# Performance work log

Hardware: AMD Instinct MI355X
Metric: run time of the kernel (lower is better)

## Reference

```python
import jax, jax.numpy as jnp
import numpy as np

NU, NI = 4000, 4000
R, M, OUT = 5, 256, 75
SIDE, FDIM = 64, 128


def setup_inputs() -> dict:
    key = jax.random.key(0)
    ks = jax.random.split(key, 12)
    return {
        "adj_matrix": jax.random.randint(ks[0], (NU, NI), 0, 6, dtype=jnp.int32),
        "u_sideFeat": jax.random.normal(ks[1], (NU, FDIM), dtype=jnp.float32),
        "v_sideFeat": jax.random.normal(ks[2], (NI, FDIM), dtype=jnp.float32),
        "msg_W": jax.random.normal(ks[3], (R, M, NU + NI), dtype=jnp.float32) * 0.05,
        "dense_W": jax.random.normal(ks[4], (OUT, M), dtype=jnp.float32) * 0.05,
        "u_W1": jax.random.normal(ks[5], (SIDE, FDIM), dtype=jnp.float32) * 0.05,
        "u_b1": jax.random.normal(ks[6], (SIDE,), dtype=jnp.float32) * 0.05,
        "u_W2": jax.random.normal(ks[7], (OUT, SIDE), dtype=jnp.float32) * 0.05,
        "v_W1": jax.random.normal(ks[8], (SIDE, FDIM), dtype=jnp.float32) * 0.05,
        "v_b1": jax.random.normal(ks[9], (SIDE,), dtype=jnp.float32) * 0.05,
        "v_W2": jax.random.normal(ks[10], (OUT, SIDE), dtype=jnp.float32) * 0.05,
        "isNegative": 0,
    }


def reference(adj_matrix, u_sideFeat, v_sideFeat, msg_W, dense_W,
              u_W1, u_b1, u_W2, v_W1, v_b1, v_W2, isNegative):
    # isNegative=0, dropout=0 -> one-hot matrices are exact identity slices,
    # so msgLayer(sum_j adj_r[i,j]/C * onehot_j) == (adj_r/C) @ W_r[:, cols].T
    nu, ni = adj_matrix.shape
    r_vals = jnp.arange(1, msg_W.shape[0] + 1, dtype=adj_matrix.dtype)
    # rating-split binary adjacencies [R, NU, NI]
    A = (adj_matrix[None, :, :] == r_vals[:, None, None]).astype(jnp.float32)
    Nu = A.sum(axis=(0, 2))            # user degree over all ratings [NU]
    Nv = A.sum(axis=(0, 1))            # item degree [NI]
    C = jnp.sqrt(Nu[:, None] * Nv[None, :])  # symmetric normalization [NU, NI]
    Csafe = jnp.where(C > 0, C, 1.0)
    An = A / Csafe[None, :, :]
    W_users = msg_W[:, :, :nu]         # [R, M, NU]
    W_items = msg_W[:, :, nu:]         # [R, M, NI]
    # accum='sum' over ratings, then relu
    Hu = jax.nn.relu(jnp.einsum('rui,rmi->um', An, W_items))  # [NU, M]
    Hv = jax.nn.relu(jnp.einsum('rui,rmu->im', An, W_users))  # [NI, M]
    Fu = jax.nn.relu(u_sideFeat @ u_W1.T + u_b1)
    Fv = jax.nn.relu(v_sideFeat @ v_W1.T + v_b1)
    U = jax.nn.relu(Hu @ dense_W.T + Fu @ u_W2.T)
    V = jax.nn.relu(Hv @ dense_W.T + Fv @ v_W2.T)
    return (U, V)
```

## Files before the change

### kernel.cpp

```cpp
#include <hip/hip_runtime.h>
#include <hip/hip_bf16.h>
#include <stdint.h>

#define NU 4000
#define NI 4000
#define RR 5
#define MM 256
#define OUTD 75
#define FDIM 128
#define KP 4096
#define KPH 2048
#define HP_STRIDE 1024000

typedef float f32x4 __attribute__((ext_vector_type(4)));
typedef int   i32x4 __attribute__((ext_vector_type(4)));
typedef short bf16x8 __attribute__((ext_vector_type(8)));

static __device__ __forceinline__ short f2b(float x) {
  __hip_bfloat16 h = __float2bfloat16(x);
  return (short)__builtin_bit_cast(unsigned short, h);
}
static __device__ __forceinline__ float b2f(short x) {
  unsigned int u = ((unsigned int)(unsigned short)x) << 16;
  return __builtin_bit_cast(float, u);
}
static __device__ __forceinline__ bf16x8 cvt8(f32x4 a, f32x4 b) {
  bf16x8 r;
  r[0] = f2b(a[0]); r[1] = f2b(a[1]); r[2] = f2b(a[2]); r[3] = f2b(a[3]);
  r[4] = f2b(b[0]); r[5] = f2b(b[1]); r[6] = f2b(b[2]); r[7] = f2b(b[3]);
  return r;
}

__global__ __launch_bounds__(256) void k_trans(const int* __restrict__ adj,
                                               uint8_t* __restrict__ a8p,
                                               uint8_t* __restrict__ a8tp,
                                               int* __restrict__ Nu,
                                               int* __restrict__ Nv) {
  __shared__ int8_t lt[64][65];
  __shared__ int rowc[64];
  __shared__ int colp[4][64];
  const int i0 = blockIdx.x * 64;
  const int u0 = blockIdx.y * 64;
  const int t = threadIdx.x;
  const int w = t >> 6, lane = t & 63;
  int mycol = 0;
  for (int rep = 0; rep < 16; rep++) {
    const int r = rep * 4 + w;
    const int u = u0 + r, i = i0 + lane;
    int a = (u < NU && i < NI) ? adj[(size_t)u * NI + i] : 0;
    const int nz = (a > 0) ? 1 : 0;
    unsigned long long bal = __ballot(nz);
    if (lane == 0) rowc[r] = (int)__popcll(bal);
    mycol += nz;
    lt[lane][r] = (int8_t)a;
    const int nb = __shfl_down(a, 1);
    if (!(lane & 1))
      a8p[(size_t)u * KPH + (i0 >> 1) + (lane >> 1)] = (uint8_t)(a | (nb << 4));
  }
  colp[w][lane] = mycol;
  __syncthreads();
  for (int rep = 0; rep < 16; rep++) {
    const int r = rep * 4 + w;
    const int it = i0 + r;
    const int v = lt[r][lane];
    const int nb = __shfl_down(v, 1);
    if (!(lane & 1))
      a8tp[(size_t)it * KPH + (u0 >> 1) + (lane >> 1)] = (uint8_t)(v | (nb << 4));
  }
  if (t < 64) {
    const int cc = colp[0][t] + colp[1][t] + colp[2][t] + colp[3][t];
    if (i0 + t < NI && cc) atomicAdd(&Nv[i0 + t], cc);
    if (u0 + t < NU && rowc[t]) atomicAdd(&Nu[u0 + t], rowc[t]);
  }
}

__global__ __launch_bounds__(256) void k_pbuild(const float* __restrict__ msgW,
                                                const int* __restrict__ Nu,
                                                const int* __restrict__ Nv,
                                                int8_t* __restrict__ Pu,
                                                int8_t* __restrict__ Pv) {
  const int b = blockIdx.x;
  const float* src = msgW + (size_t)b * (NU + NI);
#pragma unroll
  for (int it = 0; it < 2; ++it) {
    const int base = (threadIdx.x + it * 256) * 8;
    uint32_t lou = 0, hiu = 0, lov = 0, hiv = 0;
    if (base < NU) {
      const f32x4 v0 = *(const f32x4*)(src + base);
      const f32x4 v1 = *(const f32x4*)(src + base + 4);
      const f32x4 u0 = *(const f32x4*)(src + NU + base);
      const f32x4 u1 = *(const f32x4*)(src + NU + base + 4);
      const int4 cu0 = *(const int4*)(Nu + base);
      const int4 cu1 = *(const int4*)(Nu + base + 4);
      const int4 cv0 = *(const int4*)(Nv + base);
      const int4 cv1 = *(const int4*)(Nv + base + 4);
      float qv[8], qu[8];
      const int cus[8] = {cu0.x, cu0.y, cu0.z, cu0.w, cu1.x, cu1.y, cu1.z, cu1.w};
      const int cvs[8] = {cv0.x, cv0.y, cv0.z, cv0.w, cv1.x, cv1.y, cv1.z, cv1.w};
      const float vs[8] = {v0[0], v0[1], v0[2], v0[3], v1[0], v1[1], v1[2], v1[3]};
      const float us[8] = {u0[0], u0[1], u0[2], u0[3], u1[0], u1[1], u1[2], u1[3]};
#pragma unroll
      for (int j = 0; j < 8; ++j) {
        const float su = cus[j] > 0 ? rsqrtf((float)cus[j]) * 256.0f : 0.f;
        const float sv = cvs[j] > 0 ? rsqrtf((float)cvs[j]) * 256.0f : 0.f;
        qv[j] = fminf(fmaxf(vs[j] * su, -127.f), 127.f);
        qu[j] = fminf(fmaxf(us[j] * sv, -127.f), 127.f);
      }
      uint32_t bv[8], bu[8];
#pragma unroll
      for (int j = 0; j < 8; ++j) {
        bv[j] = (uint32_t)(uint8_t)(int8_t)__float2int_rn(qv[j]);
        bu[j] = (uint32_t)(uint8_t)(int8_t)__float2int_rn(qu[j]);
      }
      lov = bv[0] | (bv[2] << 8) | (bv[4] << 16) | (bv[6] << 24);
      hiv = bv[1] | (bv[3] << 8) | (bv[5] << 16) | (bv[7] << 24);
      lou = bu[0] | (bu[2] << 8) | (bu[4] << 16) | (bu[6] << 24);
      hiu = bu[1] | (bu[3] << 8) | (bu[5] << 16) | (bu[7] << 24);
    }
    *(uint2*)(Pv + (size_t)b * KP + base) = make_uint2(lov, hiv);
    *(uint2*)(Pu + (size_t)b * KP + base) = make_uint2(lou, hiu);
  }
}

#define GLOAD_LDS(g, s) __builtin_amdgcn_global_load_lds( \
    (const __attribute__((address_space(1))) uint32_t*)(g), \
    (__attribute__((address_space(3))) uint32_t*)(s), 16, 0, 0)

static __device__ __forceinline__ uint32_t ohp(uint32_t sel, int r) {
  const uint32_t TL[5] = {0x00000100u, 0x00010000u, 0x01000000u, 0u, 0u};
  const uint32_t TH[5] = {0u, 0u, 0u, 0x00000001u, 0x00000100u};
  return __builtin_amdgcn_perm(TH[r], TL[r], sel);
}

__global__ __launch_bounds__(256, 5) void k_gemm(const uint8_t* __restrict__ Au,
                                                 const uint8_t* __restrict__ Av,
                                                 const int8_t* __restrict__ Pu,
                                                 const int8_t* __restrict__ Pv,
                                                 const int* __restrict__ Nu,
                                                 const int* __restrict__ Nv,
                                                 __hip_bfloat16* __restrict__ Hp) {
  __shared__ __attribute__((aligned(16))) char Bls[2][10240];

  const int bid = blockIdx.x;
  const int side = bid & 1;
  const int bn = (bid >> 1) & 7;
  const int rest = bid >> 4;
  const int ks = rest % 5;
  const int bm = rest / 5;
  const uint8_t* __restrict__ A8 = side ? Av : Au;
  const int8_t* __restrict__ P  = side ? Pv : Pu;
  const int* __restrict__ cnt = side ? Nv : Nu;
  const int kbeg = ks * 832;
  const int nst = (ks == 4) ? 12 : 13;

  const int t = threadIdx.x;
  const int w = t >> 6, l = t & 63;
  const int l15 = l & 15, l4 = l >> 4;

  const int scnt = (w < 2) ? 3 : 2;
  const int nb = (w < 2) ? w * 3 : 6 + (w - 2) * 2;
  uint32_t soff[3], ldst[3];
  {
    const uint32_t jsrc = (uint32_t)((l & 3) ^ ((l >> 3) & 3));
#pragma unroll
    for (int i = 0; i < 3; ++i) {
      const int n = nb + ((i < scnt) ? i : 0);
      const int r = n >> 1, chunk = n & 1;
      const int colg = bn * 32 + chunk * 16 + (l >> 2);
      soff[i] = (uint32_t)(r * 256 + colg) * KP + jsrc * 16u;
      ldst[i] = (uint32_t)(n << 10);
    }
  }
#define STAGE(bi, kk) { \
  GLOAD_LDS(P + soff[0] + (uint32_t)(kk), &Bls[bi][0] + ldst[0]); \
  GLOAD_LDS(P + soff[1] + (uint32_t)(kk), &Bls[bi][0] + ldst[1]); \
  if (scnt == 3) GLOAD_LDS(P + soff[2] + (uint32_t)(kk), &Bls[bi][0] + ldst[2]); }

  const uint32_t rbase = (uint32_t)(l15 * 64) +
                         ((uint32_t)(l4 ^ ((l15 >> 1) & 3)) << 4);

  uint32_t paoff[4];
#pragma unroll
  for (int g = 0; g < 4; ++g)
    paoff[g] = (uint32_t)(bm * 256 + w * 64 + g * 16 + l15) * KPH + l4 * 8;

  i32x4 acc[4][2] = {};
  uint2 aC[4], aN[4];

  STAGE(0, kbeg);
#pragma unroll
  for (int g = 0; g < 4; ++g)
    aC[g] = *(const uint2*)(A8 + paoff[g] + (kbeg >> 1));
  __syncthreads();

  for (int st = 0; st < nst; ++st) {
    const int kk = kbeg + st * 64;
    if (st + 1 < nst) {
      STAGE((st & 1) ^ 1, kk + 64);
#pragma unroll
      for (int g = 0; g < 4; ++g)
        aN[g] = *(const uint2*)(A8 + paoff[g] + ((kk + 64) >> 1));
    }
    uint32_t ud[4][4];
#pragma unroll
    for (int g = 0; g < 4; ++g) {
      ud[g][0] = aC[g].x & 0x0F0F0F0Fu;
      ud[g][1] = (aC[g].x >> 4) & 0x0F0F0F0Fu;
      ud[g][2] = aC[g].y & 0x0F0F0F0Fu;
      ud[g][3] = (aC[g].y >> 4) & 0x0F0F0F0Fu;
    }
    const char* lb = &Bls[st & 1][0];
#pragma unroll
    for (int r = 0; r < 5; ++r) {
      const uint4 B0 = *(const uint4*)(lb + r * 2048 + rbase);
      const uint4 B1 = *(const uint4*)(lb + r * 2048 + rbase + 1024);
#pragma unroll
      for (int g = 0; g < 4; ++g) {
        uint4 af;
        af.x = ohp(ud[g][0], r); af.y = ohp(ud[g][1], r);
        af.z = ohp(ud[g][2], r); af.w = ohp(ud[g][3], r);
        const i32x4 a4 = __builtin_bit_cast(i32x4, af);
        acc[g][0] = __builtin_amdgcn_mfma_i32_16x16x64_i8(
            a4, __builtin_bit_cast(i32x4, B0), acc[g][0], 0, 0, 0);
        acc[g][1] = __builtin_amdgcn_mfma_i32_16x16x64_i8(
            a4, __builtin_bit_cast(i32x4, B1), acc[g][1], 0, 0, 0);
      }
    }
#pragma unroll
    for (int g = 0; g < 4; ++g) aC[g] = aN[g];
    __syncthreads();
  }

  __hip_bfloat16* hp = Hp + (size_t)(ks * 2 + side) * HP_STRIDE;
#pragma unroll
  for (int g = 0; g < 4; ++g) {
    const int rowb = bm * 256 + w * 64 + g * 16 + l4 * 4;
#pragma unroll
    for (int c = 0; c < 2; ++c) {
      const int ocol = bn * 32 + c * 16 + l15;
#pragma unroll
      for (int q = 0; q < 4; ++q) {
        const int orow = rowb + q;
        if (orow < 4000) {
          const int cv = cnt[orow];
          const float s = cv > 0 ? rsqrtf((float)cv) * (1.0f / 256.0f) : 0.f;
          hp[(size_t)orow * 256 + ocol] = __float2bfloat16((float)acc[g][c][q] * s);
        }
      }
    }
  }
#undef STAGE
}

__global__ __launch_bounds__(64) void k_out(const __hip_bfloat16* __restrict__ Hp,
                                            const float* __restrict__ usf,
                                            const float* __restrict__ vsf,
                                            const float* __restrict__ dW,
                                            const float* __restrict__ uW1,
                                            const float* __restrict__ ub1,
                                            const float* __restrict__ uW2,
                                            const float* __restrict__ vW1,
                                            const float* __restrict__ vb1,
                                            const float* __restrict__ vW2,
                                            float* __restrict__ out) {
  const int bid = blockIdx.x;
  const int side = bid / 250, rb = bid % 250;
  const int l = threadIdx.x & 63;
  const int l15 = l & 15, l4 = l >> 4;
  const int r0 = rb * 16;
  const float* __restrict__ sf = side ? vsf : usf;
  const float* __restrict__ W1 = side ? vW1 : uW1;
  const float* __restrict__ b1 = side ? vb1 : ub1;
  const float* __restrict__ W2 = side ? vW2 : uW2;
  const __hip_bfloat16* __restrict__ hp = Hp + (size_t)side * HP_STRIDE;

  const int myrow = r0 + l15;

  __shared__ __hip_bfloat16 lf[16][72];

  f32x4 fA[4] = {};
#pragma unroll
  for (int kk = 0; kk < 128; kk += 32) {
    const float* ps = sf + (size_t)myrow * 128 + kk + 8 * l4;
    const bf16x8 af = cvt8(*(const f32x4*)ps, *(const f32x4*)(ps + 4));
#pragma unroll
    for (int c = 0; c < 4; ++c) {
      const float* pw = W1 + (size_t)(c * 16 + l15) * 128 + kk + 8 * l4;
      const bf16x8 bf = cvt8(*(const f32x4*)pw, *(const f32x4*)(pw + 4));
      fA[c] = __builtin_amdgcn_mfma_f32_16x16x32_bf16(af, bf, fA[c], 0, 0, 0);
    }
  }
#pragma unroll
  for (int c = 0; c < 4; ++c) {
    const float bv = b1[c * 16 + l15];
#pragma unroll
    for (int reg = 0; reg < 4; ++reg) {
      float v = fA[c][reg] + bv;
      lf[l4 * 4 + reg][c * 16 + l15] = __float2bfloat16(v > 0.f ? v : 0.f);
    }
  }
  __syncthreads();

  f32x4 oA[5] = {};
  const __hip_bfloat16* hbase = hp + (size_t)myrow * 256 + 8 * l4;
#pragma unroll
  for (int kk = 0; kk < 256; kk += 32) {
    const bf16x8 q0 = *(const bf16x8*)(hbase + kk);
    const bf16x8 q1 = *(const bf16x8*)(hbase + 2 * HP_STRIDE + kk);
    const bf16x8 q2 = *(const bf16x8*)(hbase + 4 * HP_STRIDE + kk);
    const bf16x8 q3 = *(const bf16x8*)(hbase + 6 * HP_STRIDE + kk);
    const bf16x8 q4 = *(const bf16x8*)(hbase + 8 * HP_STRIDE + kk);
    bf16x8 af;
#pragma unroll
    for (int j = 0; j < 8; ++j) {
      float hv = b2f(q0[j]) + b2f(q1[j]) + b2f(q2[j]) + b2f(q3[j]) + b2f(q4[j]);
      af[j] = f2b(hv > 0.f ? hv : 0.f);
    }
#pragma unroll
    for (int c = 0; c < 5; ++c) {
      int oc = c * 16 + l15; if (oc > 74) oc = 74;
      const float* pd = dW + (size_t)oc * 256 + kk + 8 * l4;
      const bf16x8 bf = cvt8(*(const f32x4*)pd, *(const f32x4*)(pd + 4));
      oA[c] = __builtin_amdgcn_mfma_f32_16x16x32_bf16(af, bf, oA[c], 0, 0, 0);
    }
  }
#pragma unroll
  for (int kk = 0; kk < 64; kk += 32) {
    const bf16x8 af = *(const bf16x8*)(&lf[l15][kk + 8 * l4]);
#pragma unroll
    for (int c = 0; c < 5; ++c) {
      int oc = c * 16 + l15; if (oc > 74) oc = 74;
      const float* pw = W2 + (size_t)oc * 64 + kk + 8 * l4;
      const bf16x8 bf = cvt8(*(const f32x4*)pw, *(const f32x4*)(pw + 4));
      oA[c] = __builtin_amdgcn_mfma_f32_16x16x32_bf16(af, bf, oA[c], 0, 0, 0);
    }
  }
  float* po = out + (size_t)side * (4000 * 75);
#pragma unroll
  for (int c = 0; c < 5; ++c) {
    const int oc = c * 16 + l15;
    if (oc < 75) {
#pragma unroll
      for (int reg = 0; reg < 4; ++reg) {
        const int orow = r0 + l4 * 4 + reg;
        const float v = oA[c][reg];
        po[(size_t)orow * 75 + oc] = v > 0.f ? v : 0.f;
      }
    }
  }
}

extern "C" void kernel_launch(void* const* d_in, const int* in_sizes, int n_in,
                              void* d_out, int out_size, void* d_ws, size_t ws_size,
                              hipStream_t stream) {
  const int* adj = (const int*)d_in[0];
  const float* usf = (const float*)d_in[1];
  const float* vsf = (const float*)d_in[2];
  const float* msgW = (const float*)d_in[3];
  const float* dW = (const float*)d_in[4];
  const float* uW1 = (const float*)d_in[5];
  const float* ub1 = (const float*)d_in[6];
  const float* uW2 = (const float*)d_in[7];
  const float* vW1 = (const float*)d_in[8];
  const float* vb1 = (const float*)d_in[9];
  const float* vW2 = (const float*)d_in[10];
  float* out = (float*)d_out;

  char* w = (char*)d_ws;
  const size_t A_BYTES = (size_t)4096 * KPH;
  const size_t P_BYTES = (size_t)RR * MM * KP;
  const size_t HP_BYTES = (size_t)10 * HP_STRIDE * 2;
  int* Nu = (int*)w;
  int* Nv = (int*)(w + 16384);
  uint8_t* Au = (uint8_t*)(w + 32768);
  uint8_t* Av = Au + A_BYTES;
  int8_t* Pu = (int8_t*)(w + 32768 + 2 * A_BYTES);
  int8_t* Pv = Pu + P_BYTES;
  __hip_bfloat16* Hp = (__hip_bfloat16*)(w + 32768 + 2 * A_BYTES + 2 * P_BYTES);
  const size_t need = 32768 + 2 * A_BYTES + 2 * P_BYTES + HP_BYTES;
  if (ws_size < need) return;

  hipMemsetAsync(w, 0, 32768, stream);
  k_trans<<<dim3(64, 64), 256, 0, stream>>>(adj, Au, Av, Nu, Nv);
  k_pbuild<<<1280, 256, 0, stream>>>(msgW, Nu, Nv, Pu, Pv);
  k_gemm<<<1280, 256, 0, stream>>>(Au, Av, Pu, Pv, Nu, Nv, Hp);
  k_out<<<500, 64, 0, stream>>>(Hp, usf, vsf, dW, uW1, ub1, uW2, vW1, vb1, vW2,
                                out);
}
```

Baseline: 103.5 us.

## Switch int8 GEMM to 32x32x32 MFMA and split K six ways

The adjacency GEMM now uses 32x32x32 int8 MFMA tiles instead of 16x16x64, with a matching LDS staging layout and fragment mapping. The K dimension is split into six partitions instead of five, which raises the grid to 1536 blocks, and the output kernel sums six partial buffers. The larger MFMA shape is meant to cut instruction count and LDS reads per FLOP, and the extra split is meant to fill more CUs. In exchange it uses more workspace, writes and reads one more partial buffer, and unpacks the bf16 fragments differently.

```diff
diff --git a/kernel.cpp b/kernel.cpp
--- a/kernel.cpp
+++ b/kernel.cpp
@@ -14,6 +14,7 @@
 
 typedef float f32x4 __attribute__((ext_vector_type(4)));
 typedef int   i32x4 __attribute__((ext_vector_type(4)));
+typedef int   i32x16 __attribute__((ext_vector_type(16)));
 typedef short bf16x8 __attribute__((ext_vector_type(8)));
 
 static __device__ __forceinline__ short f2b(float x) {
@@ -132,7 +133,7 @@
   return __builtin_amdgcn_perm(TH[r], TL[r], sel);
 }
 
-__global__ __launch_bounds__(256, 5) void k_gemm(const uint8_t* __restrict__ Au,
+__global__ __launch_bounds__(256, 6) void k_gemm(const uint8_t* __restrict__ Au,
                                                  const uint8_t* __restrict__ Av,
                                                  const int8_t* __restrict__ Pu,
                                                  const int8_t* __restrict__ Pv,
@@ -145,52 +146,49 @@
   const int side = bid & 1;
   const int bn = (bid >> 1) & 7;
   const int rest = bid >> 4;
-  const int ks = rest % 5;
-  const int bm = rest / 5;
+  const int ks = rest % 6;
+  const int bm = rest / 6;
   const uint8_t* __restrict__ A8 = side ? Av : Au;
   const int8_t* __restrict__ P  = side ? Pv : Pu;
   const int* __restrict__ cnt = side ? Nv : Nu;
-  const int kbeg = ks * 832;
-  const int nst = (ks == 4) ? 12 : 13;
+  const int kbeg = (ks < 4) ? ks * 704 : 2816 + (ks - 4) * 640;
+  const int nst = (ks < 4) ? 11 : 10;
 
   const int t = threadIdx.x;
   const int w = t >> 6, l = t & 63;
-  const int l15 = l & 15, l4 = l >> 4;
+  const int l31 = l & 31, lh = l >> 5;
 
   const int scnt = (w < 2) ? 3 : 2;
   const int nb = (w < 2) ? w * 3 : 6 + (w - 2) * 2;
   uint32_t soff[3], ldst[3];
-  {
-    const uint32_t jsrc = (uint32_t)((l & 3) ^ ((l >> 3) & 3));
-#pragma unroll
-    for (int i = 0; i < 3; ++i) {
-      const int n = nb + ((i < scnt) ? i : 0);
-      const int r = n >> 1, chunk = n & 1;
-      const int colg = bn * 32 + chunk * 16 + (l >> 2);
-      soff[i] = (uint32_t)(r * 256 + colg) * KP + jsrc * 16u;
-      ldst[i] = (uint32_t)(n << 10);
-    }
+#pragma unroll
+  for (int i = 0; i < 3; ++i) {
+    const int n = nb + ((i < scnt) ? i : 0);
+    const int r = n >> 1, h = n & 1;
+    soff[i] = (uint32_t)((r * 256 + bn * 32 + l31) * KP) +
+              (uint32_t)(lh * 32 + h * 16);
+    ldst[i] = (uint32_t)(n << 10);
   }
 #define STAGE(bi, kk) { \
   GLOAD_LDS(P + soff[0] + (uint32_t)(kk), &Bls[bi][0] + ldst[0]); \
   GLOAD_LDS(P + soff[1] + (uint32_t)(kk), &Bls[bi][0] + ldst[1]); \
   if (scnt == 3) GLOAD_LDS(P + soff[2] + (uint32_t)(kk), &Bls[bi][0] + ldst[2]); }
 
-  const uint32_t rbase = (uint32_t)(l15 * 64) +
-                         ((uint32_t)(l4 ^ ((l15 >> 1) & 3)) << 4);
-
-  uint32_t paoff[4];
-#pragma unroll
-  for (int g = 0; g < 4; ++g)
-    paoff[g] = (uint32_t)(bm * 256 + w * 64 + g * 16 + l15) * KPH + l4 * 8;
-
-  i32x4 acc[4][2] = {};
-  uint2 aC[4], aN[4];
+  const uint32_t rb2 = (uint32_t)(lh * 512 + l31 * 16);
+
+  uint32_t paoff[2];
+#pragma unroll
+  for (int g = 0; g < 2; ++g)
+    paoff[g] = (uint32_t)(bm * 256 + w * 64 + g * 32 + l31) * KPH + lh * 16;
+
+  i32x16 acc[2] = {};
+  uint4 aC[2], aN[2];
 
   STAGE(0, kbeg);
 #pragma unroll
-  for (int g = 0; g < 4; ++g)
-    aC[g] = *(const uint2*)(A8 + paoff[g] + (kbeg >> 1));
+  for (int g = 0; g < 2; ++g)
+    aC[g] = *(const uint4*)(A8 + paoff[g] + (kbeg >> 1));
+  aN[0] = aC[0]; aN[1] = aC[1];
   __syncthreads();
 
   for (int st = 0; st < nst; ++st) {
@@ -198,54 +196,57 @@
     if (st + 1 < nst) {
       STAGE((st & 1) ^ 1, kk + 64);
 #pragma unroll
-      for (int g = 0; g < 4; ++g)
-        aN[g] = *(const uint2*)(A8 + paoff[g] + ((kk + 64) >> 1));
-    }
-    uint32_t ud[4][4];
-#pragma unroll
-    for (int g = 0; g < 4; ++g) {
+      for (int g = 0; g < 2; ++g)
+        aN[g] = *(const uint4*)(A8 + paoff[g] + ((kk + 64) >> 1));
+    }
+    uint32_t ud[2][8];
+#pragma unroll
+    for (int g = 0; g < 2; ++g) {
       ud[g][0] = aC[g].x & 0x0F0F0F0Fu;
       ud[g][1] = (aC[g].x >> 4) & 0x0F0F0F0Fu;
       ud[g][2] = aC[g].y & 0x0F0F0F0Fu;
       ud[g][3] = (aC[g].y >> 4) & 0x0F0F0F0Fu;
+      ud[g][4] = aC[g].z & 0x0F0F0F0Fu;
+      ud[g][5] = (aC[g].z >> 4) & 0x0F0F0F0Fu;
+      ud[g][6] = aC[g].w & 0x0F0F0F0Fu;
+      ud[g][7] = (aC[g].w >> 4) & 0x0F0F0F0Fu;
     }
     const char* lb = &Bls[st & 1][0];
 #pragma unroll
     for (int r = 0; r < 5; ++r) {
-      const uint4 B0 = *(const uint4*)(lb + r * 2048 + rbase);
-      const uint4 B1 = *(const uint4*)(lb + r * 2048 + rbase + 1024);
-#pragma unroll
-      for (int g = 0; g < 4; ++g) {
-        uint4 af;
-        af.x = ohp(ud[g][0], r); af.y = ohp(ud[g][1], r);
-        af.z = ohp(ud[g][2], r); af.w = ohp(ud[g][3], r);
-        const i32x4 a4 = __builtin_bit_cast(i32x4, af);
-        acc[g][0] = __builtin_amdgcn_mfma_i32_16x16x64_i8(
-            a4, __builtin_bit_cast(i32x4, B0), acc[g][0], 0, 0, 0);
-        acc[g][1] = __builtin_amdgcn_mfma_i32_16x16x64_i8(
-            a4, __builtin_bit_cast(i32x4, B1), acc[g][1], 0, 0, 0);
-      }
-    }
-#pragma unroll
-    for (int g = 0; g < 4; ++g) aC[g] = aN[g];
+      const uint4 B0 = *(const uint4*)(lb + r * 2048 + rb2);
+      const uint4 B1 = *(const uint4*)(lb + r * 2048 + 1024 + rb2);
+#pragma unroll
+      for (int g = 0; g < 2; ++g) {
+        uint4 a0, a1;
+        a0.x = ohp(ud[g][0], r); a0.y = ohp(ud[g][1], r);
+        a0.z = ohp(ud[g][2], r); a0.w = ohp(ud[g][3], r);
+        acc[g] = __builtin_amdgcn_mfma_i32_32x32x32_i8(
+            __builtin_bit_cast(i32x4, a0), __builtin_bit_cast(i32x4, B0),
+            acc[g], 0, 0, 0);
+        a1.x = ohp(ud[g][4], r); a1.y = ohp(ud[g][5], r);
+        a1.z = ohp(ud[g][6], r); a1.w = ohp(ud[g][7], r);
+        acc[g] = __builtin_amdgcn_mfma_i32_32x32x32_i8(
+            __builtin_bit_cast(i32x4, a1), __builtin_bit_cast(i32x4, B1),
+            acc[g], 0, 0, 0);
+      }
+    }
+    aC[0] = aN[0]; aC[1] = aN[1];
     __syncthreads();
   }
 
   __hip_bfloat16* hp = Hp + (size_t)(ks * 2 + side) * HP_STRIDE;
-#pragma unroll
-  for (int g = 0; g < 4; ++g) {
-    const int rowb = bm * 256 + w * 64 + g * 16 + l4 * 4;
-#pragma unroll
-    for (int c = 0; c < 2; ++c) {
-      const int ocol = bn * 32 + c * 16 + l15;
-#pragma unroll
-      for (int q = 0; q < 4; ++q) {
-        const int orow = rowb + q;
-        if (orow < 4000) {
-          const int cv = cnt[orow];
-          const float s = cv > 0 ? rsqrtf((float)cv) * (1.0f / 256.0f) : 0.f;
-          hp[(size_t)orow * 256 + ocol] = __float2bfloat16((float)acc[g][c][q] * s);
-        }
+  const int ocol = bn * 32 + l31;
+#pragma unroll
+  for (int g = 0; g < 2; ++g) {
+    const int rowb = bm * 256 + w * 64 + g * 32 + 4 * lh;
+#pragma unroll
+    for (int reg = 0; reg < 16; ++reg) {
+      const int orow = rowb + (reg & 3) + 8 * (reg >> 2);
+      if (orow < 4000) {
+        const int cv = cnt[orow];
+        const float s = cv > 0 ? rsqrtf((float)cv) * (1.0f / 256.0f) : 0.f;
+        hp[(size_t)orow * 256 + ocol] = __float2bfloat16((float)acc[g][reg] * s);
       }
     }
   }
@@ -310,10 +311,12 @@
     const bf16x8 q2 = *(const bf16x8*)(hbase + 4 * HP_STRIDE + kk);
     const bf16x8 q3 = *(const bf16x8*)(hbase + 6 * HP_STRIDE + kk);
     const bf16x8 q4 = *(const bf16x8*)(hbase + 8 * HP_STRIDE + kk);
+    const bf16x8 q5 = *(const bf16x8*)(hbase + 10 * HP_STRIDE + kk);
     bf16x8 af;
 #pragma unroll
     for (int j = 0; j < 8; ++j) {
-      float hv = b2f(q0[j]) + b2f(q1[j]) + b2f(q2[j]) + b2f(q3[j]) + b2f(q4[j]);
+      float hv = b2f(q0[j]) + b2f(q1[j]) + b2f(q2[j]) + b2f(q3[j]) +
+                 b2f(q4[j]) + b2f(q5[j]);
       af[j] = f2b(hv > 0.f ? hv : 0.f);
     }
 #pragma unroll
@@ -369,7 +372,7 @@
   char* w = (char*)d_ws;
   const size_t A_BYTES = (size_t)4096 * KPH;
   const size_t P_BYTES = (size_t)RR * MM * KP;
-  const size_t HP_BYTES = (size_t)10 * HP_STRIDE * 2;
+  const size_t HP_BYTES = (size_t)12 * HP_STRIDE * 2;
   int* Nu = (int*)w;
   int* Nv = (int*)(w + 16384);
   uint8_t* Au = (uint8_t*)(w + 32768);
@@ -383,7 +386,7 @@
   hipMemsetAsync(w, 0, 32768, stream);
   k_trans<<<dim3(64, 64), 256, 0, stream>>>(adj, Au, Av, Nu, Nv);
   k_pbuild<<<1280, 256, 0, stream>>>(msgW, Nu, Nv, Pu, Pv);
-  k_gemm<<<1280, 256, 0, stream>>>(Au, Av, Pu, Pv, Nu, Nv, Hp);
+  k_gemm<<<1536, 256, 0, stream>>>(Au, Av, Pu, Pv, Nu, Nv, Hp);
   k_out<<<500, 64, 0, stream>>>(Hp, usf, vsf, dW, uW1, ub1, uW2, vW1, vb1, vW2,
                                 out);
 }
```

Result: slower. 110.2 us (+6.5%).

## Vectorize nibble packing in transpose and split output kernel across four waves

Applied to the files above, without the earlier changes.

The transpose kernel now stages both the row and transposed tiles in shared memory and packs nibbles with wide 32-bit perm operations and 8-byte stores, replacing per-lane shuffles and byte stores. A new pre-kernel converts the dense and side-feature weights to bf16 once, with padded rows, so the output kernel no longer converts fp32 weights inside its loops. The output kernel moves from one wave per 16 rows to four waves per 32 rows. The side-feature MLP and half of the dense K-loop run concurrently in separate waves, and the partial sums are combined through shared memory. This adds a launch, two barriers and extra shared memory in exchange for better overlap and occupancy in the small tail stages.

```diff
diff --git a/kernel.cpp b/kernel.cpp
--- a/kernel.cpp
+++ b/kernel.cpp
@@ -36,7 +36,8 @@
                                                uint8_t* __restrict__ a8tp,
                                                int* __restrict__ Nu,
                                                int* __restrict__ Nv) {
-  __shared__ int8_t lt[64][65];
+  __shared__ int8_t lp[64][68];
+  __shared__ int8_t lt[64][68];
   __shared__ int rowc[64];
   __shared__ int colp[4][64];
   const int i0 = blockIdx.x * 64;
@@ -52,20 +53,26 @@
     unsigned long long bal = __ballot(nz);
     if (lane == 0) rowc[r] = (int)__popcll(bal);
     mycol += nz;
+    lp[r][lane] = (int8_t)a;
     lt[lane][r] = (int8_t)a;
-    const int nb = __shfl_down(a, 1);
-    if (!(lane & 1))
-      a8p[(size_t)u * KPH + (i0 >> 1) + (lane >> 1)] = (uint8_t)(a | (nb << 4));
   }
   colp[w][lane] = mycol;
   __syncthreads();
-  for (int rep = 0; rep < 16; rep++) {
-    const int r = rep * 4 + w;
-    const int it = i0 + r;
-    const int v = lt[r][lane];
-    const int nb = __shfl_down(v, 1);
-    if (!(lane & 1))
-      a8tp[(size_t)it * KPH + (u0 >> 1) + (lane >> 1)] = (uint8_t)(v | (nb << 4));
+  {
+    const int r = t >> 2, c = t & 3;
+    const uint32_t* xp = (const uint32_t*)(&lp[r][c * 16]);
+    const uint32_t* xt = (const uint32_t*)(&lt[r][c * 16]);
+    uint32_t t0, t1, t2, t3, w0, w1;
+    t0 = xp[0] | (xp[0] >> 4); t1 = xp[1] | (xp[1] >> 4);
+    t2 = xp[2] | (xp[2] >> 4); t3 = xp[3] | (xp[3] >> 4);
+    w0 = __builtin_amdgcn_perm(t1, t0, 0x06040200u);
+    w1 = __builtin_amdgcn_perm(t3, t2, 0x06040200u);
+    *(uint2*)(a8p + (size_t)(u0 + r) * KPH + (i0 >> 1) + c * 8) = make_uint2(w0, w1);
+    t0 = xt[0] | (xt[0] >> 4); t1 = xt[1] | (xt[1] >> 4);
+    t2 = xt[2] | (xt[2] >> 4); t3 = xt[3] | (xt[3] >> 4);
+    w0 = __builtin_amdgcn_perm(t1, t0, 0x06040200u);
+    w1 = __builtin_amdgcn_perm(t3, t2, 0x06040200u);
+    *(uint2*)(a8tp + (size_t)(i0 + r) * KPH + (u0 >> 1) + c * 8) = make_uint2(w0, w1);
   }
   if (t < 64) {
     const int cc = colp[0][t] + colp[1][t] + colp[2][t] + colp[3][t];
@@ -122,6 +129,32 @@
   }
 }
 
+__global__ __launch_bounds__(256) void k_wcvt(const float* __restrict__ dW,
+                                              const float* __restrict__ uW1,
+                                              const float* __restrict__ vW1,
+                                              const float* __restrict__ uW2,
+                                              const float* __restrict__ vW2,
+                                              __hip_bfloat16* __restrict__ dWb,
+                                              __hip_bfloat16* __restrict__ W1b,
+                                              __hip_bfloat16* __restrict__ W2b) {
+  const int tid = blockIdx.x * 256 + threadIdx.x;
+  const int stride = gridDim.x * 256;
+  for (int idx = tid; idx < 80 * 256; idx += stride) {
+    const int oc = idx >> 8, k = idx & 255;
+    dWb[idx] = __float2bfloat16(oc < 75 ? dW[oc * 256 + k] : 0.f);
+  }
+  for (int idx = tid; idx < 2 * 64 * 128; idx += stride) {
+    const int s = idx >> 13, r = idx & 8191;
+    W1b[idx] = __float2bfloat16(s ? vW1[r] : uW1[r]);
+  }
+  for (int idx = tid; idx < 2 * 80 * 64; idx += stride) {
+    const int s = idx / 5120, r = idx % 5120;
+    const int oc = r >> 6, k = r & 63;
+    const float* W2 = s ? vW2 : uW2;
+    W2b[idx] = __float2bfloat16(oc < 75 ? W2[oc * 64 + k] : 0.f);
+  }
+}
+
 #define GLOAD_LDS(g, s) __builtin_amdgcn_global_load_lds( \
     (const __attribute__((address_space(1))) uint32_t*)(g), \
     (__attribute__((address_space(3))) uint32_t*)(s), 16, 0, 0)
@@ -252,102 +285,115 @@
 #undef STAGE
 }
 
-__global__ __launch_bounds__(64) void k_out(const __hip_bfloat16* __restrict__ Hp,
-                                            const float* __restrict__ usf,
-                                            const float* __restrict__ vsf,
-                                            const float* __restrict__ dW,
-                                            const float* __restrict__ uW1,
-                                            const float* __restrict__ ub1,
-                                            const float* __restrict__ uW2,
-                                            const float* __restrict__ vW1,
-                                            const float* __restrict__ vb1,
-                                            const float* __restrict__ vW2,
-                                            float* __restrict__ out) {
+__global__ __launch_bounds__(256) void k_out(const __hip_bfloat16* __restrict__ Hp,
+                                             const float* __restrict__ usf,
+                                             const float* __restrict__ vsf,
+                                             const __hip_bfloat16* __restrict__ dWb,
+                                             const __hip_bfloat16* __restrict__ W1b,
+                                             const float* __restrict__ ub1,
+                                             const float* __restrict__ vb1,
+                                             const __hip_bfloat16* __restrict__ W2b,
+                                             float* __restrict__ out) {
   const int bid = blockIdx.x;
-  const int side = bid / 250, rb = bid % 250;
-  const int l = threadIdx.x & 63;
+  const int side = bid / 125, rb = bid % 125;
+  const int t = threadIdx.x, w = t >> 6, l = t & 63;
+  const int rowg = w >> 1, kh = w & 1;
   const int l15 = l & 15, l4 = l >> 4;
-  const int r0 = rb * 16;
   const float* __restrict__ sf = side ? vsf : usf;
-  const float* __restrict__ W1 = side ? vW1 : uW1;
   const float* __restrict__ b1 = side ? vb1 : ub1;
-  const float* __restrict__ W2 = side ? vW2 : uW2;
+  const __hip_bfloat16* __restrict__ W1 = W1b + side * (64 * 128);
+  const __hip_bfloat16* __restrict__ W2 = W2b + side * (80 * 64);
   const __hip_bfloat16* __restrict__ hp = Hp + (size_t)side * HP_STRIDE;
-
+  const int r0 = rb * 32 + rowg * 16;
   const int myrow = r0 + l15;
 
-  __shared__ __hip_bfloat16 lf[16][72];
-
-  f32x4 fA[4] = {};
-#pragma unroll
-  for (int kk = 0; kk < 128; kk += 32) {
-    const float* ps = sf + (size_t)myrow * 128 + kk + 8 * l4;
-    const bf16x8 af = cvt8(*(const f32x4*)ps, *(const f32x4*)(ps + 4));
-#pragma unroll
-    for (int c = 0; c < 4; ++c) {
-      const float* pw = W1 + (size_t)(c * 16 + l15) * 128 + kk + 8 * l4;
-      const bf16x8 bf = cvt8(*(const f32x4*)pw, *(const f32x4*)(pw + 4));
-      fA[c] = __builtin_amdgcn_mfma_f32_16x16x32_bf16(af, bf, fA[c], 0, 0, 0);
-    }
-  }
-#pragma unroll
-  for (int c = 0; c < 4; ++c) {
-    const float bv = b1[c * 16 + l15];
-#pragma unroll
-    for (int reg = 0; reg < 4; ++reg) {
-      float v = fA[c][reg] + bv;
-      lf[l4 * 4 + reg][c * 16 + l15] = __float2bfloat16(v > 0.f ? v : 0.f);
-    }
-  }
-  __syncthreads();
+  __shared__ __hip_bfloat16 lf[2][16][72];
+  __shared__ float ps[2][80][20];
 
   f32x4 oA[5] = {};
   const __hip_bfloat16* hbase = hp + (size_t)myrow * 256 + 8 * l4;
-#pragma unroll
-  for (int kk = 0; kk < 256; kk += 32) {
-    const bf16x8 q0 = *(const bf16x8*)(hbase + kk);
-    const bf16x8 q1 = *(const bf16x8*)(hbase + 2 * HP_STRIDE + kk);
-    const bf16x8 q2 = *(const bf16x8*)(hbase + 4 * HP_STRIDE + kk);
-    const bf16x8 q3 = *(const bf16x8*)(hbase + 6 * HP_STRIDE + kk);
-    const bf16x8 q4 = *(const bf16x8*)(hbase + 8 * HP_STRIDE + kk);
-    bf16x8 af;
-#pragma unroll
-    for (int j = 0; j < 8; ++j) {
-      float hv = b2f(q0[j]) + b2f(q1[j]) + b2f(q2[j]) + b2f(q3[j]) + b2f(q4[j]);
-      af[j] = f2b(hv > 0.f ? hv : 0.f);
-    }
+
+#define PHASE_B_HALF(kb) { \
+  _Pragma("unroll") \
+  for (int i_ = 0; i_ < 4; ++i_) { \
+    const int kk_ = (kb) + i_ * 32; \
+    const bf16x8 q0 = *(const bf16x8*)(hbase + kk_); \
+    const bf16x8 q1 = *(const bf16x8*)(hbase + 2 * HP_STRIDE + kk_); \
+    const bf16x8 q2 = *(const bf16x8*)(hbase + 4 * HP_STRIDE + kk_); \
+    const bf16x8 q3 = *(const bf16x8*)(hbase + 6 * HP_STRIDE + kk_); \
+    const bf16x8 q4 = *(const bf16x8*)(hbase + 8 * HP_STRIDE + kk_); \
+    bf16x8 af; \
+    _Pragma("unroll") \
+    for (int j_ = 0; j_ < 8; ++j_) { \
+      float hv = b2f(q0[j_]) + b2f(q1[j_]) + b2f(q2[j_]) + b2f(q3[j_]) + b2f(q4[j_]); \
+      af[j_] = f2b(hv > 0.f ? hv : 0.f); \
+    } \
+    _Pragma("unroll") \
+    for (int c_ = 0; c_ < 5; ++c_) { \
+      const bf16x8 bf = *(const bf16x8*)(dWb + (c_ * 16 + l15) * 256 + kk_ + 8 * l4); \
+      oA[c_] = __builtin_amdgcn_mfma_f32_16x16x32_bf16(af, bf, oA[c_], 0, 0, 0); \
+    } \
+  } }
+
+  if (kh == 0) {
+    f32x4 fA[4] = {};
+#pragma unroll
+    for (int kk = 0; kk < 128; kk += 32) {
+      const float* psf = sf + (size_t)myrow * 128 + kk + 8 * l4;
+      const bf16x8 af = cvt8(*(const f32x4*)psf, *(const f32x4*)(psf + 4));
+#pragma unroll
+      for (int c = 0; c < 4; ++c) {
+        const bf16x8 bf = *(const bf16x8*)(W1 + (c * 16 + l15) * 128 + kk + 8 * l4);
+        fA[c] = __builtin_amdgcn_mfma_f32_16x16x32_bf16(af, bf, fA[c], 0, 0, 0);
+      }
+    }
+#pragma unroll
+    for (int c = 0; c < 4; ++c) {
+      const float bv = b1[c * 16 + l15];
+#pragma unroll
+      for (int reg = 0; reg < 4; ++reg) {
+        float v = fA[c][reg] + bv;
+        lf[rowg][l4 * 4 + reg][c * 16 + l15] = __float2bfloat16(v > 0.f ? v : 0.f);
+      }
+    }
+  } else {
+    PHASE_B_HALF(128)
+  }
+  __syncthreads();
+  if (kh == 0) {
+    PHASE_B_HALF(0)
+  } else {
+#pragma unroll
+    for (int kk = 0; kk < 64; kk += 32) {
+      const bf16x8 af = *(const bf16x8*)(&lf[rowg][l15][kk + 8 * l4]);
+#pragma unroll
+      for (int c = 0; c < 5; ++c) {
+        const bf16x8 bf = *(const bf16x8*)(W2 + (c * 16 + l15) * 64 + kk + 8 * l4);
+        oA[c] = __builtin_amdgcn_mfma_f32_16x16x32_bf16(af, bf, oA[c], 0, 0, 0);
+      }
+    }
+#pragma unroll
+    for (int c = 0; c < 5; ++c)
+      *(f32x4*)&ps[rowg][c * 16 + l15][l4 * 4] = oA[c];
+  }
+  __syncthreads();
+  if (kh == 0) {
+    float* po = out + (size_t)side * (4000 * 75);
 #pragma unroll
     for (int c = 0; c < 5; ++c) {
-      int oc = c * 16 + l15; if (oc > 74) oc = 74;
-      const float* pd = dW + (size_t)oc * 256 + kk + 8 * l4;
-      const bf16x8 bf = cvt8(*(const f32x4*)pd, *(const f32x4*)(pd + 4));
-      oA[c] = __builtin_amdgcn_mfma_f32_16x16x32_bf16(af, bf, oA[c], 0, 0, 0);
-    }
-  }
-#pragma unroll
-  for (int kk = 0; kk < 64; kk += 32) {
-    const bf16x8 af = *(const bf16x8*)(&lf[l15][kk + 8 * l4]);
-#pragma unroll
-    for (int c = 0; c < 5; ++c) {
-      int oc = c * 16 + l15; if (oc > 74) oc = 74;
-      const float* pw = W2 + (size_t)oc * 64 + kk + 8 * l4;
-      const bf16x8 bf = cvt8(*(const f32x4*)pw, *(const f32x4*)(pw + 4));
-      oA[c] = __builtin_amdgcn_mfma_f32_16x16x32_bf16(af, bf, oA[c], 0, 0, 0);
-    }
-  }
-  float* po = out + (size_t)side * (4000 * 75);
-#pragma unroll
-  for (int c = 0; c < 5; ++c) {
-    const int oc = c * 16 + l15;
-    if (oc < 75) {
-#pragma unroll
-      for (int reg = 0; reg < 4; ++reg) {
-        const int orow = r0 + l4 * 4 + reg;
-        const float v = oA[c][reg];
-        po[(size_t)orow * 75 + oc] = v > 0.f ? v : 0.f;
-      }
-    }
-  }
+      const int oc = c * 16 + l15;
+      if (oc < 75) {
+        const f32x4 pv = *(const f32x4*)&ps[rowg][oc][l4 * 4];
+#pragma unroll
+        for (int reg = 0; reg < 4; ++reg) {
+          const int orow = r0 + l4 * 4 + reg;
+          const float v = oA[c][reg] + pv[reg];
+          po[(size_t)orow * 75 + oc] = v > 0.f ? v : 0.f;
+        }
+      }
+    }
+  }
+#undef PHASE_B_HALF
 }
 
 extern "C" void kernel_launch(void* const* d_in, const int* in_sizes, int n_in,
@@ -377,13 +423,17 @@
   int8_t* Pu = (int8_t*)(w + 32768 + 2 * A_BYTES);
   int8_t* Pv = Pu + P_BYTES;
   __hip_bfloat16* Hp = (__hip_bfloat16*)(w + 32768 + 2 * A_BYTES + 2 * P_BYTES);
-  const size_t need = 32768 + 2 * A_BYTES + 2 * P_BYTES + HP_BYTES;
+  char* wb = (char*)(Hp) + HP_BYTES;
+  __hip_bfloat16* dWb = (__hip_bfloat16*)wb;
+  __hip_bfloat16* W1b = (__hip_bfloat16*)(wb + 40960);
+  __hip_bfloat16* W2b = (__hip_bfloat16*)(wb + 40960 + 32768);
+  const size_t need = 32768 + 2 * A_BYTES + 2 * P_BYTES + HP_BYTES + 94208;
   if (ws_size < need) return;
 
   hipMemsetAsync(w, 0, 32768, stream);
+  k_wcvt<<<64, 256, 0, stream>>>(dW, uW1, vW1, uW2, vW2, dWb, W1b, W2b);
   k_trans<<<dim3(64, 64), 256, 0, stream>>>(adj, Au, Av, Nu, Nv);
   k_pbuild<<<1280, 256, 0, stream>>>(msgW, Nu, Nv, Pu, Pv);
   k_gemm<<<1280, 256, 0, stream>>>(Au, Av, Pu, Pv, Nu, Nv, Hp);
-  k_out<<<500, 64, 0, stream>>>(Hp, usf, vsf, dW, uW1, ub1, uW2, vW1, vb1, vW2,
-                                out);
-}
+  k_out<<<250, 256, 0, stream>>>(Hp, usf, vsf, dWb, W1b, ub1, vb1, W2b, out);
+}
```

Result: no change. 102.0 us (-1.5%).
